# Kernel tuning notes

Hardware: AMD Instinct MI355X
Metric: run time of the kernel (lower is better)

## Reference

```python
import jax, jax.numpy as jnp
import numpy as np

FEATURE_DIM = 32

def setup_inputs() -> dict:
    key = jax.random.key(0)
    k_pts, k_w1, k_b1, k_w2, k_b2 = jax.random.split(key, 5)
    B, N = 4096, 4096
    points = jax.random.normal(k_pts, (B, N, 2), dtype=jnp.float32)
    # torch Linear default init: U(-1/sqrt(fan_in), 1/sqrt(fan_in))
    lim1 = 1.0 / np.sqrt(10.0)
    lim2 = 1.0 / np.sqrt(64.0)
    W1 = jax.random.uniform(k_w1, (10, 64), minval=-lim1, maxval=lim1, dtype=jnp.float32)
    b1 = jax.random.uniform(k_b1, (64,), minval=-lim1, maxval=lim1, dtype=jnp.float32)
    W2 = jax.random.uniform(k_w2, (64, FEATURE_DIM), minval=-lim2, maxval=lim2, dtype=jnp.float32)
    b2 = jax.random.uniform(k_b2, (FEATURE_DIM,), minval=-lim2, maxval=lim2, dtype=jnp.float32)
    return {"points": points, "W1": W1, "b1": b1, "W2": W2, "b2": b2}

def _geo_features(points):
    # points: (B, N, 2) -> (B, 10)
    bbox_min = jnp.min(points, axis=1)            # (B, 2)
    bbox_max = jnp.max(points, axis=1)            # (B, 2)
    bbox_center = (bbox_min + bbox_max) * 0.5
    bbox_size = bbox_max - bbox_min
    centroid = jnp.mean(points, axis=1)           # (B, 2)
    std = jnp.std(points, axis=1)                 # population std (ddof=0), matches np.std
    diffs = points - centroid[:, None, :]         # (B, N, 2)
    distances = jnp.linalg.norm(diffs, axis=2)    # (B, N)
    dist_mean = jnp.mean(distances, axis=1)       # (B,)
    dist_std = jnp.std(distances, axis=1)         # (B,)
    return jnp.concatenate(
        [bbox_center, bbox_size, centroid, std, dist_mean[:, None], dist_std[:, None]],
        axis=1,
    )  # (B, 10)

def reference(points, W1, b1, W2, b2):
    geo = _geo_features(points)                   # (B, 10)
    h = jax.nn.relu(geo @ W1 + b1)                # (B, 64)
    return jax.nn.relu(h @ W2 + b2)               # (B, feature_dim)
```

## Files before the change

### kernel.cpp

```cpp
#include <hip/hip_runtime.h>
#include <math.h>

#define NPTS 4096
#define BLOCK 256
#define PTS4 (NPTS / 2)
#define ITERS (PTS4 / BLOCK)

__global__ __launch_bounds__(BLOCK) void geo_mlp_kernel(
    const float* __restrict__ points,
    const float* __restrict__ W1,
    const float* __restrict__ b1,
    const float* __restrict__ W2,
    const float* __restrict__ b2,
    float* __restrict__ out)
{
    __shared__ float4 pts[PTS4];
    __shared__ float wred[4][10];
    __shared__ float h[64];

    const int tid  = threadIdx.x;
    const int lane = tid & 63;
    const int wave = tid >> 6;
    const int b    = blockIdx.x;

    const float4* __restrict__ src =
        (const float4*)(points + (size_t)b * NPTS * 2);

    float minx =  INFINITY, miny =  INFINITY;
    float maxx = -INFINITY, maxy = -INFINITY;
    float sx = 0.f, sy = 0.f, sxx = 0.f, syy = 0.f;

    #pragma unroll
    for (int i = 0; i < ITERS; ++i) {
        const int idx = tid + i * BLOCK;
        float4 v = src[idx];
        pts[idx] = v;
        minx = fminf(minx, fminf(v.x, v.z));
        maxx = fmaxf(maxx, fmaxf(v.x, v.z));
        miny = fminf(miny, fminf(v.y, v.w));
        maxy = fmaxf(maxy, fmaxf(v.y, v.w));
        sx += v.x + v.z;
        sy += v.y + v.w;
        sxx = fmaf(v.x, v.x, sxx); sxx = fmaf(v.z, v.z, sxx);
        syy = fmaf(v.y, v.y, syy); syy = fmaf(v.w, v.w, syy);
    }

    #pragma unroll
    for (int off = 32; off > 0; off >>= 1) {
        minx = fminf(minx, __shfl_down(minx, off));
        maxx = fmaxf(maxx, __shfl_down(maxx, off));
        miny = fminf(miny, __shfl_down(miny, off));
        maxy = fmaxf(maxy, __shfl_down(maxy, off));
        sx  += __shfl_down(sx,  off);
        sy  += __shfl_down(sy,  off);
        sxx += __shfl_down(sxx, off);
        syy += __shfl_down(syy, off);
    }
    if (lane == 0) {
        wred[wave][0] = minx; wred[wave][1] = maxx;
        wred[wave][2] = miny; wred[wave][3] = maxy;
        wred[wave][4] = sx;   wred[wave][5] = sy;
        wred[wave][6] = sxx;  wred[wave][7] = syy;
    }
    __syncthreads();

    float fminx = fminf(fminf(wred[0][0], wred[1][0]), fminf(wred[2][0], wred[3][0]));
    float fmaxx = fmaxf(fmaxf(wred[0][1], wred[1][1]), fmaxf(wred[2][1], wred[3][1]));
    float fminy = fminf(fminf(wred[0][2], wred[1][2]), fminf(wred[2][2], wred[3][2]));
    float fmaxy = fmaxf(fmaxf(wred[0][3], wred[1][3]), fmaxf(wred[2][3], wred[3][3]));
    float fsx  = (wred[0][4] + wred[1][4]) + (wred[2][4] + wred[3][4]);
    float fsy  = (wred[0][5] + wred[1][5]) + (wred[2][5] + wred[3][5]);
    float fsxx = (wred[0][6] + wred[1][6]) + (wred[2][6] + wred[3][6]);
    float fsyy = (wred[0][7] + wred[1][7]) + (wred[2][7] + wred[3][7]);

    const float invN = 1.0f / (float)NPTS;
    const float cx = fsx * invN;
    const float cy = fsy * invN;

    float sd = 0.f, sd2 = 0.f;
    #pragma unroll
    for (int i = 0; i < ITERS; ++i) {
        float4 v = pts[tid + i * BLOCK];
        float dx0 = v.x - cx, dy0 = v.y - cy;
        float dx1 = v.z - cx, dy1 = v.w - cy;
        float d0 = sqrtf(fmaf(dx0, dx0, dy0 * dy0));
        float d1 = sqrtf(fmaf(dx1, dx1, dy1 * dy1));
        sd += d0 + d1;
        sd2 = fmaf(d0, d0, sd2);
        sd2 = fmaf(d1, d1, sd2);
    }
    #pragma unroll
    for (int off = 32; off > 0; off >>= 1) {
        sd  += __shfl_down(sd,  off);
        sd2 += __shfl_down(sd2, off);
    }
    if (lane == 0) {
        wred[wave][8] = sd;
        wred[wave][9] = sd2;
    }
    __syncthreads();

    if (tid < 64) {
        float fsd  = (wred[0][8] + wred[1][8]) + (wred[2][8] + wred[3][8]);
        float fsd2 = (wred[0][9] + wred[1][9]) + (wred[2][9] + wred[3][9]);
        float dist_mean = fsd * invN;
        float dist_std  = sqrtf(fmaxf(fsd2 * invN - dist_mean * dist_mean, 0.f));
        float stdx = sqrtf(fmaxf(fsxx * invN - cx * cx, 0.f));
        float stdy = sqrtf(fmaxf(fsyy * invN - cy * cy, 0.f));

        float g[10];
        g[0] = (fminx + fmaxx) * 0.5f;
        g[1] = (fminy + fmaxy) * 0.5f;
        g[2] = fmaxx - fminx;
        g[3] = fmaxy - fminy;
        g[4] = cx;
        g[5] = cy;
        g[6] = stdx;
        g[7] = stdy;
        g[8] = dist_mean;
        g[9] = dist_std;

        float acc = b1[tid];
        #pragma unroll
        for (int i = 0; i < 10; ++i)
            acc = fmaf(g[i], W1[i * 64 + tid], acc);
        h[tid] = fmaxf(acc, 0.f);
    }
    __syncthreads();

    if (tid < 32) {
        float acc = b2[tid];
        #pragma unroll
        for (int i = 0; i < 64; ++i)
            acc = fmaf(h[i], W2[i * 32 + tid], acc);
        out[(size_t)b * 32 + tid] = fmaxf(acc, 0.f);
    }
}

extern "C" void kernel_launch(void* const* d_in, const int* in_sizes, int n_in,
                              void* d_out, int out_size, void* d_ws, size_t ws_size,
                              hipStream_t stream) {
    const float* points = (const float*)d_in[0];
    const float* W1     = (const float*)d_in[1];
    const float* b1     = (const float*)d_in[2];
    const float* W2     = (const float*)d_in[3];
    const float* b2     = (const float*)d_in[4];
    float* out          = (float*)d_out;

    const int B = in_sizes[0] / (NPTS * 2);
    geo_mlp_kernel<<<B, BLOCK, 0, stream>>>(points, W1, b1, W2, b2, out);
}
```

Before: 30.92 us.

## Keep points in registers instead of LDS and derive distance variance algebraically

The 32 KB LDS staging buffer is replaced by 8 float4 registers per thread, so the second pass reads registers instead of shared memory and LDS no longer limits blocks per CU. Launch bounds now request 8 blocks per SM. The sum of squared distances is computed from the existing sxx+syy moments rather than accumulated separately, which removes one accumulator and one reduction. This uses more registers per thread, and the E[d^2] from raw moments may lose some precision through cancellation.

```diff
diff --git a/kernel.cpp b/kernel.cpp
--- a/kernel.cpp
+++ b/kernel.cpp
@@ -6,7 +6,7 @@
 #define PTS4 (NPTS / 2)
 #define ITERS (PTS4 / BLOCK)
 
-__global__ __launch_bounds__(BLOCK) void geo_mlp_kernel(
+__global__ __launch_bounds__(BLOCK, 8) void geo_mlp_kernel(
     const float* __restrict__ points,
     const float* __restrict__ W1,
     const float* __restrict__ b1,
@@ -14,8 +14,7 @@
     const float* __restrict__ b2,
     float* __restrict__ out)
 {
-    __shared__ float4 pts[PTS4];
-    __shared__ float wred[4][10];
+    __shared__ float wred[4][9];
     __shared__ float h[64];
 
     const int tid  = threadIdx.x;
@@ -26,15 +25,18 @@
     const float4* __restrict__ src =
         (const float4*)(points + (size_t)b * NPTS * 2);
 
+    float4 p[ITERS];
+    #pragma unroll
+    for (int i = 0; i < ITERS; ++i)
+        p[i] = src[tid + i * BLOCK];
+
     float minx =  INFINITY, miny =  INFINITY;
     float maxx = -INFINITY, maxy = -INFINITY;
     float sx = 0.f, sy = 0.f, sxx = 0.f, syy = 0.f;
 
     #pragma unroll
     for (int i = 0; i < ITERS; ++i) {
-        const int idx = tid + i * BLOCK;
-        float4 v = src[idx];
-        pts[idx] = v;
+        float4 v = p[i];
         minx = fminf(minx, fminf(v.x, v.z));
         maxx = fmaxf(maxx, fmaxf(v.x, v.z));
         miny = fminf(miny, fminf(v.y, v.w));
@@ -77,34 +79,27 @@
     const float cx = fsx * invN;
     const float cy = fsy * invN;
 
-    float sd = 0.f, sd2 = 0.f;
+    float sd = 0.f;
     #pragma unroll
     for (int i = 0; i < ITERS; ++i) {
-        float4 v = pts[tid + i * BLOCK];
+        float4 v = p[i];
         float dx0 = v.x - cx, dy0 = v.y - cy;
         float dx1 = v.z - cx, dy1 = v.w - cy;
-        float d0 = sqrtf(fmaf(dx0, dx0, dy0 * dy0));
-        float d1 = sqrtf(fmaf(dx1, dx1, dy1 * dy1));
-        sd += d0 + d1;
-        sd2 = fmaf(d0, d0, sd2);
-        sd2 = fmaf(d1, d1, sd2);
+        sd += sqrtf(fmaf(dx0, dx0, dy0 * dy0));
+        sd += sqrtf(fmaf(dx1, dx1, dy1 * dy1));
     }
     #pragma unroll
-    for (int off = 32; off > 0; off >>= 1) {
-        sd  += __shfl_down(sd,  off);
-        sd2 += __shfl_down(sd2, off);
-    }
-    if (lane == 0) {
+    for (int off = 32; off > 0; off >>= 1)
+        sd += __shfl_down(sd, off);
+    if (lane == 0)
         wred[wave][8] = sd;
-        wred[wave][9] = sd2;
-    }
     __syncthreads();
 
     if (tid < 64) {
         float fsd  = (wred[0][8] + wred[1][8]) + (wred[2][8] + wred[3][8]);
-        float fsd2 = (wred[0][9] + wred[1][9]) + (wred[2][9] + wred[3][9]);
         float dist_mean = fsd * invN;
-        float dist_std  = sqrtf(fmaxf(fsd2 * invN - dist_mean * dist_mean, 0.f));
+        float ed2 = (fsxx + fsyy) * invN - (cx * cx + cy * cy);
+        float dist_std  = sqrtf(fmaxf(ed2 - dist_mean * dist_mean, 0.f));
         float stdx = sqrtf(fmaxf(fsxx * invN - cx * cx, 0.f));
         float stdy = sqrtf(fmaxf(fsyy * invN - cy * cy, 0.f));
 
```

Result: no change. 31.06 us (+0.4%).
